# Kernel tuning notes

Hardware: AMD Instinct MI355X
Metric: run time of the kernel (lower is better)

Reference implementation:

```python
import jax, jax.numpy as jnp
import numpy as np

N_NODES = 50000
N_EDGES = 800000
NUM_FEATURES = 128
HIDDEN = 128


def _gcn_conv(x, src, dst, norm, W, b, num_nodes):
    # x: [N, F_in], W: [F_in, F_out]
    h = x @ W                              # dense transform first (PyG order)
    msg = h[src] * norm[:, None]           # gather + per-edge scale
    out = jax.ops.segment_sum(msg, dst, num_segments=num_nodes)  # scatter-add
    return out + b


def _prep_edges(edge_index, num_nodes):
    # add self loops
    loop = jnp.arange(num_nodes, dtype=edge_index.dtype)
    src = jnp.concatenate([edge_index[0], loop])
    dst = jnp.concatenate([edge_index[1], loop])
    # symmetric normalization deg^{-1/2}[src] * deg^{-1/2}[dst]
    deg = jax.ops.segment_sum(jnp.ones_like(dst, dtype=jnp.float32), dst,
                              num_segments=num_nodes)
    dinv = jnp.where(deg > 0, jax.lax.rsqrt(deg), 0.0)
    norm = dinv[src] * dinv[dst]
    return src, dst, norm


def setup_inputs() -> dict:
    key = jax.random.key(0)
    ks = jax.random.split(key, 5)
    s1 = 1.0 / np.sqrt(NUM_FEATURES)
    s2 = 1.0 / np.sqrt(HIDDEN)
    return {
        "x": jax.random.normal(ks[0], (N_NODES, NUM_FEATURES), jnp.float32),
        "edge_index": jax.random.randint(ks[1], (2, N_EDGES), 0, N_NODES,
                                         dtype=jnp.int64),
        "W1": jax.random.normal(ks[2], (NUM_FEATURES, HIDDEN), jnp.float32) * s1,
        "b1": jnp.zeros((HIDDEN,), jnp.float32),
        "W2": jax.random.normal(ks[3], (HIDDEN, HIDDEN), jnp.float32) * s2,
        "b2": jnp.zeros((HIDDEN,), jnp.float32),
        "Wout": jax.random.normal(ks[4], (HIDDEN, 1), jnp.float32) * s2,
        "bout": jnp.zeros((1,), jnp.float32),
    }


def reference(x, edge_index, W1, b1, W2, b2, Wout, bout):
    num_nodes = x.shape[0]
    src, dst, norm = _prep_edges(edge_index, num_nodes)
    h = _gcn_conv(x, src, dst, norm, W1, b1, num_nodes)
    h = jax.nn.relu(h)
    h = _gcn_conv(h, src, dst, norm, W2, b2, num_nodes)
    h = jax.nn.relu(h)
    return jax.nn.sigmoid(h @ Wout + bout)
```

## Files before the change

### kernel.cpp

```cpp
#include <hip/hip_runtime.h>
#include <math.h>

#define NN 50000
#define NE 800000
#define NBUK 196
#define PBLK 256
#define EPB (NE / PBLK)

typedef __attribute__((ext_vector_type(8))) short bf16x8;
typedef __attribute__((ext_vector_type(4))) float f32x4;

__device__ __forceinline__ unsigned short f2b(float f) {
  union { float f; unsigned u; } v; v.f = f;
  unsigned r = v.u + 0x7FFF + ((v.u >> 16) & 1);
  return (unsigned short)(r >> 16);
}
__device__ __forceinline__ float plo(unsigned v) {
  union { unsigned u; float f; } t; t.u = v << 16; return t.f;
}
__device__ __forceinline__ float phi(unsigned v) {
  union { unsigned u; float f; } t; t.u = v & 0xFFFF0000u; return t.f;
}

__device__ __forceinline__ int edge_val(const void* ei, long long idx, int is64) {
  if (is64) return (int)((const long long*)ei)[idx];
  return ((const int*)ei)[idx];
}

__global__ __launch_bounds__(256) void k_phist(const void* __restrict__ ei,
                                               int* __restrict__ bh) {
  __shared__ int hist[NBUK];
  __shared__ int sflag;
  if (threadIdx.x < 64) {
    unsigned v = ((const unsigned*)ei)[2 * threadIdx.x + 1];
    unsigned long long m = __ballot(v == 0u);
    if (threadIdx.x == 0) sflag = (m == ~0ull) ? 1 : 0;
  }
  if (threadIdx.x < NBUK) hist[threadIdx.x] = 0;
  __syncthreads();
  int is64 = sflag;
  int base = blockIdx.x * EPB;
  for (int e = base + threadIdx.x; e < base + EPB; e += 256) {
    int d = edge_val(ei, (long long)NE + e, is64);
    atomicAdd(&hist[d >> 8], 1);
  }
  __syncthreads();
  if (threadIdx.x < NBUK) bh[threadIdx.x * PBLK + blockIdx.x] = hist[threadIdx.x];
}

__global__ __launch_bounds__(256) void k_pscanA(int* __restrict__ bh,
                                                int* __restrict__ colsum) {
  __shared__ int sh[256];
  int k = blockIdx.x, t = threadIdx.x;
  int v = bh[k * PBLK + t];
  sh[t] = v;
  __syncthreads();
  for (int s = 1; s < 256; s <<= 1) {
    int u = (t >= s) ? sh[t - s] : 0;
    __syncthreads();
    sh[t] += u;
    __syncthreads();
  }
  bh[k * PBLK + t] = sh[t] - v;
  if (t == 255) colsum[k] = sh[255];
}

__global__ __launch_bounds__(256) void k_pscanB(const int* __restrict__ colsum,
                                                int* __restrict__ bstart) {
  __shared__ int sh[256];
  int t = threadIdx.x;
  sh[t] = (t < NBUK) ? colsum[t] : 0;
  __syncthreads();
  for (int s = 1; s < 256; s <<= 1) {
    int u = (t >= s) ? sh[t - s] : 0;
    __syncthreads();
    sh[t] += u;
    __syncthreads();
  }
  if (t <= NBUK) bstart[t] = (t == 0) ? 0 : sh[t - 1];
}

__global__ __launch_bounds__(256) void k_pscat(const void* __restrict__ ei,
                                               const int* __restrict__ bh,
                                               const int* __restrict__ bstart,
                                               int2* __restrict__ epair) {
  __shared__ int cur[NBUK];
  __shared__ int sflag;
  if (threadIdx.x < 64) {
    unsigned v = ((const unsigned*)ei)[2 * threadIdx.x + 1];
    unsigned long long m = __ballot(v == 0u);
    if (threadIdx.x == 0) sflag = (m == ~0ull) ? 1 : 0;
  }
  if (threadIdx.x < NBUK)
    cur[threadIdx.x] = bstart[threadIdx.x] + bh[threadIdx.x * PBLK + blockIdx.x];
  __syncthreads();
  int is64 = sflag;
  int base = blockIdx.x * EPB;
  for (int e = base + threadIdx.x; e < base + EPB; e += 256) {
    int d = edge_val(ei, (long long)NE + e, is64);
    int s = edge_val(ei, e, is64);
    int p = atomicAdd(&cur[d >> 8], 1);
    epair[p] = make_int2(s, d);
  }
}

__global__ __launch_bounds__(256) void k_boff(const int2* __restrict__ epair,
                                              const int* __restrict__ bstart,
                                              int* __restrict__ off,
                                              float* __restrict__ dinv) {
  __shared__ int hist[256];
  int k = blockIdx.x, t = threadIdx.x;
  hist[t] = 0;
  __syncthreads();
  int e0 = bstart[k], e1 = bstart[k + 1];
  for (int e = e0 + t; e < e1; e += 256)
    atomicAdd(&hist[epair[e].y & 255], 1);
  __syncthreads();
  int myc = hist[t];
  for (int s = 1; s < 256; s <<= 1) {
    int u = (t >= s) ? hist[t - s] : 0;
    __syncthreads();
    hist[t] += u;
    __syncthreads();
  }
  int node = k * 256 + t;
  if (node < NN) {
    off[node] = e0 + hist[t] - myc;
    dinv[node] = rsqrtf((float)(myc + 1));
  }
  if (k == 0 && t == 0) off[NN] = NE;
}

__global__ __launch_bounds__(256) void k_bfill(const int2* __restrict__ epair,
                                               const int* __restrict__ bstart,
                                               const int* __restrict__ off,
                                               int* __restrict__ csr) {
  __shared__ int cur[256];
  int k = blockIdx.x, t = threadIdx.x;
  int node = k * 256 + t;
  cur[t] = (node < NN) ? off[node] : 0;
  __syncthreads();
  int e0 = bstart[k], e1 = bstart[k + 1];
  for (int e = e0 + t; e < e1; e += 256) {
    int2 p2 = epair[e];
    int p = atomicAdd(&cur[p2.y & 255], 1);
    csr[p] = p2.x;
  }
}

__global__ __launch_bounds__(256) void k_wt2(const float* __restrict__ W1,
                                             const float* __restrict__ W2,
                                             unsigned short* __restrict__ Wt1,
                                             unsigned short* __restrict__ Wt2) {
  int i = blockIdx.x * 256 + threadIdx.x;
  int sel = i >> 14;
  int j = i & 16383;
  int k = j >> 7, n = j & 127;
  const float* W = sel ? W2 : W1;
  unsigned short* Wt = sel ? Wt2 : Wt1;
  Wt[n * 128 + k] = f2b(W[j]);
}

template <int A_F32>
__global__ __launch_bounds__(256, 2) void k_mgemm(const void* __restrict__ Ap,
                                                  const unsigned short* __restrict__ Wt,
                                                  unsigned short* __restrict__ Out,
                                                  int M) {
  int wid  = (blockIdx.x * blockDim.x + threadIdx.x) >> 6;
  int lane = threadIdx.x & 63;
  int nw   = (gridDim.x * blockDim.x) >> 6;
  int r  = lane & 15;
  int kg = lane >> 4;
  bf16x8 wf[8][4];
#pragma unroll
  for (int n = 0; n < 8; ++n)
#pragma unroll
    for (int kk = 0; kk < 4; ++kk)
      wf[n][kk] = *(const bf16x8*)&Wt[(n * 16 + r) * 128 + kk * 32 + kg * 8];
  int nstr = M >> 4;
  for (int s = wid; s < nstr; s += nw) {
    int row = s * 16 + r;
    bf16x8 xf[4];
    if (A_F32) {
      const float* Ar = (const float*)Ap + (long long)row * 128 + kg * 8;
#pragma unroll
      for (int kk = 0; kk < 4; ++kk) {
        float4 lo4 = *(const float4*)(Ar + kk * 32);
        float4 hi4 = *(const float4*)(Ar + kk * 32 + 4);
        bf16x8 t;
        t[0] = (short)f2b(lo4.x); t[1] = (short)f2b(lo4.y);
        t[2] = (short)f2b(lo4.z); t[3] = (short)f2b(lo4.w);
        t[4] = (short)f2b(hi4.x); t[5] = (short)f2b(hi4.y);
        t[6] = (short)f2b(hi4.z); t[7] = (short)f2b(hi4.w);
        xf[kk] = t;
      }
    } else {
      const unsigned short* Ar = (const unsigned short*)Ap + (long long)row * 128 + kg * 8;
#pragma unroll
      for (int kk = 0; kk < 4; ++kk)
        xf[kk] = *(const bf16x8*)(Ar + kk * 32);
    }
    f32x4 acc[8];
#pragma unroll
    for (int n = 0; n < 8; ++n) acc[n] = (f32x4){0.f, 0.f, 0.f, 0.f};
#pragma unroll
    for (int kk = 0; kk < 4; ++kk)
#pragma unroll
      for (int n = 0; n < 8; ++n)
        acc[n] = __builtin_amdgcn_mfma_f32_16x16x32_bf16(wf[n][kk], xf[kk], acc[n], 0, 0, 0);
    unsigned short* Or = Out + (long long)row * 128 + kg * 4;
#pragma unroll
    for (int n = 0; n < 8; ++n) {
      uint2 o;
      o.x = (unsigned)f2b(acc[n][0]) | ((unsigned)f2b(acc[n][1]) << 16);
      o.y = (unsigned)f2b(acc[n][2]) | ((unsigned)f2b(acc[n][3]) << 16);
      *(uint2*)(Or + n * 16) = o;
    }
  }
}

template <int FINAL>
__global__ __launch_bounds__(256) void k_agg(const unsigned short* __restrict__ Tb,
                                             const int* __restrict__ off,
                                             const int* __restrict__ csr,
                                             const float* __restrict__ dinv,
                                             const float* __restrict__ bias,
                                             const float* __restrict__ wout,
                                             const float* __restrict__ bout,
                                             void* __restrict__ outp) {
  const unsigned* Tw = (const unsigned*)Tb;
  int wid  = (blockIdx.x * blockDim.x + threadIdx.x) >> 6;
  int lane = threadIdx.x & 63;
  int nw   = (gridDim.x * blockDim.x) >> 6;
  float blo = bias[2 * lane], bhi = bias[2 * lane + 1];
  float wlo = 0.f, whi = 0.f;
  if (FINAL) { wlo = wout[2 * lane]; whi = wout[2 * lane + 1]; }
  for (int d = wid; d < NN; d += nw) {
    float dv = dinv[d];
    int e0 = off[d], e1 = off[d + 1];
    unsigned vs = Tw[d * 64 + lane];
    float a0 = dv * plo(vs);
    float a1 = dv * phi(vs);
    int e = e0;
    int e8 = e0 + ((e1 - e0) & ~7);
    for (; e < e8; e += 8) {
      int   si[8]; float wi[8]; unsigned vi[8];
#pragma unroll
      for (int q = 0; q < 8; ++q) si[q] = csr[e + q];
#pragma unroll
      for (int q = 0; q < 8; ++q) wi[q] = dinv[si[q]];
#pragma unroll
      for (int q = 0; q < 8; ++q) vi[q] = Tw[si[q] * 64 + lane];
#pragma unroll
      for (int q = 0; q < 8; ++q) {
        a0 = fmaf(wi[q], plo(vi[q]), a0);
        a1 = fmaf(wi[q], phi(vi[q]), a1);
      }
    }
    for (; e < e1; ++e) {
      int s = csr[e];
      float w = dinv[s];
      unsigned v = Tw[s * 64 + lane];
      a0 = fmaf(w, plo(v), a0);
      a1 = fmaf(w, phi(v), a1);
    }
    a0 = fmaxf(fmaf(a0, dv, blo), 0.f);
    a1 = fmaxf(fmaf(a1, dv, bhi), 0.f);
    if (FINAL) {
      float rsum = a0 * wlo + a1 * whi;
#pragma unroll
      for (int s2p = 32; s2p > 0; s2p >>= 1) rsum += __shfl_xor(rsum, s2p, 64);
      if (lane == 0) ((float*)outp)[d] = 1.f / (1.f + __expf(-(rsum + bout[0])));
    } else {
      unsigned o = (unsigned)f2b(a0) | ((unsigned)f2b(a1) << 16);
      ((unsigned*)outp)[d * 64 + lane] = o;
    }
  }
}

extern "C" void kernel_launch(void* const* d_in, const int* in_sizes, int n_in,
                              void* d_out, int out_size, void* d_ws, size_t ws_size,
                              hipStream_t stream) {
  const float* x  = (const float*)d_in[0];
  const void*  ei = d_in[1];
  const float* W1 = (const float*)d_in[2];
  const float* b1 = (const float*)d_in[3];
  const float* W2 = (const float*)d_in[4];
  const float* b2 = (const float*)d_in[5];
  const float* Wo = (const float*)d_in[6];
  const float* bo = (const float*)d_in[7];
  float* out = (float*)d_out;

  char* p = (char*)d_ws;
  auto alloc = [&](size_t bytes) {
    char* r = p;
    p += (bytes + 511) & ~(size_t)511;
    return r;
  };
  int*   bh     = (int*)alloc(sizeof(int) * NBUK * PBLK);
  int*   colsum = (int*)alloc(sizeof(int) * NBUK);
  int*   bstart = (int*)alloc(sizeof(int) * (NBUK + 1));
  int*   off    = (int*)alloc(sizeof(int) * (NN + 1));
  float* dinv   = (float*)alloc(sizeof(float) * NN);
  int*   csr    = (int*)alloc(sizeof(int) * NE);
  unsigned short* Wt1 = (unsigned short*)alloc(sizeof(short) * 128 * 128);
  unsigned short* Wt2 = (unsigned short*)alloc(sizeof(short) * 128 * 128);
  unsigned short* T   = (unsigned short*)alloc(sizeof(short) * (size_t)NN * 128);
  unsigned short* H   = (unsigned short*)alloc(sizeof(short) * (size_t)NN * 128);
  int2* epair = (int2*)T;

  k_phist<<<PBLK, 256, 0, stream>>>(ei, bh);
  k_pscanA<<<NBUK, 256, 0, stream>>>(bh, colsum);
  k_pscanB<<<1, 256, 0, stream>>>(colsum, bstart);
  k_pscat<<<PBLK, 256, 0, stream>>>(ei, bh, bstart, epair);
  k_boff<<<NBUK, 256, 0, stream>>>(epair, bstart, off, dinv);
  k_bfill<<<NBUK, 256, 0, stream>>>(epair, bstart, off, csr);
  k_wt2<<<128, 256, 0, stream>>>(W1, W2, Wt1, Wt2);

  k_mgemm<1><<<512, 256, 0, stream>>>(x, Wt1, T, NN);
  k_agg<0><<<2048, 256, 0, stream>>>(T, off, csr, dinv, b1, nullptr, nullptr, H);
  k_mgemm<0><<<512, 256, 0, stream>>>(H, Wt2, T, NN);
  k_agg<1><<<2048, 256, 0, stream>>>(T, off, csr, dinv, b2, Wo, bo, out);
}
```

Measured before the change: 241.7 us.

## Pre-scale GEMM rows by dinv, pack CSR to 16-bit, split aggregation across half-waves

Each GEMM output row is now multiplied by dinv[row], so aggregation no longer gathers dinv per edge. CSR indices are stored as 16-bit values, and the offset and fill kernels are merged into one, with 32-bit packed edge pairs. Aggregation processes two edges per wave, one per half-wave with 8-byte loads per lane, then combines the halves with a shuffle. The risk is that 16-bit indices cannot address all 50000 nodes, since values above 65535 would be truncated, and node ids fit only because NN < 65536.

```diff
diff --git a/kernel.cpp b/kernel.cpp
--- a/kernel.cpp
+++ b/kernel.cpp
@@ -83,7 +83,7 @@
 __global__ __launch_bounds__(256) void k_pscat(const void* __restrict__ ei,
                                                const int* __restrict__ bh,
                                                const int* __restrict__ bstart,
-                                               int2* __restrict__ epair) {
+                                               unsigned* __restrict__ epk) {
   __shared__ int cur[NBUK];
   __shared__ int sflag;
   if (threadIdx.x < 64) {
@@ -100,21 +100,23 @@
     int d = edge_val(ei, (long long)NE + e, is64);
     int s = edge_val(ei, e, is64);
     int p = atomicAdd(&cur[d >> 8], 1);
-    epair[p] = make_int2(s, d);
-  }
-}
-
-__global__ __launch_bounds__(256) void k_boff(const int2* __restrict__ epair,
-                                              const int* __restrict__ bstart,
-                                              int* __restrict__ off,
-                                              float* __restrict__ dinv) {
+    epk[p] = (unsigned)s | ((unsigned)(d & 255) << 16);
+  }
+}
+
+__global__ __launch_bounds__(256) void k_bofffill(const unsigned* __restrict__ epk,
+                                                  const int* __restrict__ bstart,
+                                                  int* __restrict__ off,
+                                                  float* __restrict__ dinv,
+                                                  unsigned short* __restrict__ csr16) {
   __shared__ int hist[256];
+  __shared__ int cur[256];
   int k = blockIdx.x, t = threadIdx.x;
   hist[t] = 0;
   __syncthreads();
   int e0 = bstart[k], e1 = bstart[k + 1];
   for (int e = e0 + t; e < e1; e += 256)
-    atomicAdd(&hist[epair[e].y & 255], 1);
+    atomicAdd(&hist[(epk[e] >> 16) & 255], 1);
   __syncthreads();
   int myc = hist[t];
   for (int s = 1; s < 256; s <<= 1) {
@@ -123,29 +125,20 @@
     hist[t] += u;
     __syncthreads();
   }
+  int excl = hist[t] - myc;
   int node = k * 256 + t;
   if (node < NN) {
-    off[node] = e0 + hist[t] - myc;
+    off[node] = e0 + excl;
     dinv[node] = rsqrtf((float)(myc + 1));
   }
+  cur[t] = e0 + excl;
+  __syncthreads();
+  for (int e = e0 + t; e < e1; e += 256) {
+    unsigned pk = epk[e];
+    int p = atomicAdd(&cur[(pk >> 16) & 255], 1);
+    csr16[p] = (unsigned short)(pk & 0xFFFFu);
+  }
   if (k == 0 && t == 0) off[NN] = NE;
-}
-
-__global__ __launch_bounds__(256) void k_bfill(const int2* __restrict__ epair,
-                                               const int* __restrict__ bstart,
-                                               const int* __restrict__ off,
-                                               int* __restrict__ csr) {
-  __shared__ int cur[256];
-  int k = blockIdx.x, t = threadIdx.x;
-  int node = k * 256 + t;
-  cur[t] = (node < NN) ? off[node] : 0;
-  __syncthreads();
-  int e0 = bstart[k], e1 = bstart[k + 1];
-  for (int e = e0 + t; e < e1; e += 256) {
-    int2 p2 = epair[e];
-    int p = atomicAdd(&cur[p2.y & 255], 1);
-    csr[p] = p2.x;
-  }
 }
 
 __global__ __launch_bounds__(256) void k_wt2(const float* __restrict__ W1,
@@ -164,6 +157,7 @@
 template <int A_F32>
 __global__ __launch_bounds__(256, 2) void k_mgemm(const void* __restrict__ Ap,
                                                   const unsigned short* __restrict__ Wt,
+                                                  const float* __restrict__ dinv,
                                                   unsigned short* __restrict__ Out,
                                                   int M) {
   int wid  = (blockIdx.x * blockDim.x + threadIdx.x) >> 6;
@@ -208,12 +202,13 @@
 #pragma unroll
       for (int n = 0; n < 8; ++n)
         acc[n] = __builtin_amdgcn_mfma_f32_16x16x32_bf16(wf[n][kk], xf[kk], acc[n], 0, 0, 0);
+    float dv = dinv[row];
     unsigned short* Or = Out + (long long)row * 128 + kg * 4;
 #pragma unroll
     for (int n = 0; n < 8; ++n) {
       uint2 o;
-      o.x = (unsigned)f2b(acc[n][0]) | ((unsigned)f2b(acc[n][1]) << 16);
-      o.y = (unsigned)f2b(acc[n][2]) | ((unsigned)f2b(acc[n][3]) << 16);
+      o.x = (unsigned)f2b(acc[n][0] * dv) | ((unsigned)f2b(acc[n][1] * dv) << 16);
+      o.y = (unsigned)f2b(acc[n][2] * dv) | ((unsigned)f2b(acc[n][3] * dv) << 16);
       *(uint2*)(Or + n * 16) = o;
     }
   }
@@ -222,58 +217,76 @@
 template <int FINAL>
 __global__ __launch_bounds__(256) void k_agg(const unsigned short* __restrict__ Tb,
                                              const int* __restrict__ off,
-                                             const int* __restrict__ csr,
+                                             const unsigned short* __restrict__ csr16,
                                              const float* __restrict__ dinv,
                                              const float* __restrict__ bias,
                                              const float* __restrict__ wout,
                                              const float* __restrict__ bout,
                                              void* __restrict__ outp) {
-  const unsigned* Tw = (const unsigned*)Tb;
+  const uint2* Tw2 = (const uint2*)Tb;
   int wid  = (blockIdx.x * blockDim.x + threadIdx.x) >> 6;
   int lane = threadIdx.x & 63;
+  int half = lane >> 5;
+  int li   = lane & 31;
   int nw   = (gridDim.x * blockDim.x) >> 6;
-  float blo = bias[2 * lane], bhi = bias[2 * lane + 1];
-  float wlo = 0.f, whi = 0.f;
-  if (FINAL) { wlo = wout[2 * lane]; whi = wout[2 * lane + 1]; }
+  float4 b4 = ((const float4*)bias)[li];
+  float4 w4 = make_float4(0.f, 0.f, 0.f, 0.f);
+  if (FINAL) w4 = ((const float4*)wout)[li];
   for (int d = wid; d < NN; d += nw) {
+    int e0 = off[d], e1 = off[d + 1];
+    int np  = (e1 - e0) >> 1;
+    int rem = (e1 - e0) & 1;
+    int s_init = half ? (rem ? (int)csr16[e1 - 1] : -1) : d;
+    float a0 = 0.f, a1 = 0.f, a2 = 0.f, a3 = 0.f;
+    if (s_init >= 0) {
+      uint2 vv = Tw2[s_init * 32 + li];
+      a0 = plo(vv.x); a1 = phi(vv.x); a2 = plo(vv.y); a3 = phi(vv.y);
+    }
+    int st = 0;
+    int base = e0 + half;
+    for (; st + 4 <= np; st += 4) {
+      int s0 = csr16[base + 2 * st];
+      int s1 = csr16[base + 2 * st + 2];
+      int s2 = csr16[base + 2 * st + 4];
+      int s3 = csr16[base + 2 * st + 6];
+      uint2 v0 = Tw2[s0 * 32 + li];
+      uint2 v1 = Tw2[s1 * 32 + li];
+      uint2 v2 = Tw2[s2 * 32 + li];
+      uint2 v3 = Tw2[s3 * 32 + li];
+      a0 += plo(v0.x); a1 += phi(v0.x); a2 += plo(v0.y); a3 += phi(v0.y);
+      a0 += plo(v1.x); a1 += phi(v1.x); a2 += plo(v1.y); a3 += phi(v1.y);
+      a0 += plo(v2.x); a1 += phi(v2.x); a2 += plo(v2.y); a3 += phi(v2.y);
+      a0 += plo(v3.x); a1 += phi(v3.x); a2 += plo(v3.y); a3 += phi(v3.y);
+    }
+    for (; st < np; ++st) {
+      int s = csr16[base + 2 * st];
+      uint2 vv = Tw2[s * 32 + li];
+      a0 += plo(vv.x); a1 += phi(vv.x); a2 += plo(vv.y); a3 += phi(vv.y);
+    }
+    a0 += __shfl_xor(a0, 32, 64);
+    a1 += __shfl_xor(a1, 32, 64);
+    a2 += __shfl_xor(a2, 32, 64);
+    a3 += __shfl_xor(a3, 32, 64);
     float dv = dinv[d];
-    int e0 = off[d], e1 = off[d + 1];
-    unsigned vs = Tw[d * 64 + lane];
-    float a0 = dv * plo(vs);
-    float a1 = dv * phi(vs);
-    int e = e0;
-    int e8 = e0 + ((e1 - e0) & ~7);
-    for (; e < e8; e += 8) {
-      int   si[8]; float wi[8]; unsigned vi[8];
-#pragma unroll
-      for (int q = 0; q < 8; ++q) si[q] = csr[e + q];
-#pragma unroll
-      for (int q = 0; q < 8; ++q) wi[q] = dinv[si[q]];
-#pragma unroll
-      for (int q = 0; q < 8; ++q) vi[q] = Tw[si[q] * 64 + lane];
-#pragma unroll
-      for (int q = 0; q < 8; ++q) {
-        a0 = fmaf(wi[q], plo(vi[q]), a0);
-        a1 = fmaf(wi[q], phi(vi[q]), a1);
+    a0 = fmaxf(fmaf(a0, dv, b4.x), 0.f);
+    a1 = fmaxf(fmaf(a1, dv, b4.y), 0.f);
+    a2 = fmaxf(fmaf(a2, dv, b4.z), 0.f);
+    a3 = fmaxf(fmaf(a3, dv, b4.w), 0.f);
+    if (FINAL) {
+      float r = a0 * w4.x + a1 * w4.y + a2 * w4.z + a3 * w4.w;
+      r += __shfl_xor(r, 16, 64);
+      r += __shfl_xor(r, 8, 64);
+      r += __shfl_xor(r, 4, 64);
+      r += __shfl_xor(r, 2, 64);
+      r += __shfl_xor(r, 1, 64);
+      if (lane == 0) ((float*)outp)[d] = 1.f / (1.f + __expf(-(r + bout[0])));
+    } else {
+      if (half == 0) {
+        uint2 o;
+        o.x = (unsigned)f2b(a0) | ((unsigned)f2b(a1) << 16);
+        o.y = (unsigned)f2b(a2) | ((unsigned)f2b(a3) << 16);
+        ((uint2*)outp)[d * 32 + li] = o;
       }
-    }
-    for (; e < e1; ++e) {
-      int s = csr[e];
-      float w = dinv[s];
-      unsigned v = Tw[s * 64 + lane];
-      a0 = fmaf(w, plo(v), a0);
-      a1 = fmaf(w, phi(v), a1);
-    }
-    a0 = fmaxf(fmaf(a0, dv, blo), 0.f);
-    a1 = fmaxf(fmaf(a1, dv, bhi), 0.f);
-    if (FINAL) {
-      float rsum = a0 * wlo + a1 * whi;
-#pragma unroll
-      for (int s2p = 32; s2p > 0; s2p >>= 1) rsum += __shfl_xor(rsum, s2p, 64);
-      if (lane == 0) ((float*)outp)[d] = 1.f / (1.f + __expf(-(rsum + bout[0])));
-    } else {
-      unsigned o = (unsigned)f2b(a0) | ((unsigned)f2b(a1) << 16);
-      ((unsigned*)outp)[d * 64 + lane] = o;
     }
   }
 }
@@ -302,23 +315,22 @@
   int*   bstart = (int*)alloc(sizeof(int) * (NBUK + 1));
   int*   off    = (int*)alloc(sizeof(int) * (NN + 1));
   float* dinv   = (float*)alloc(sizeof(float) * NN);
-  int*   csr    = (int*)alloc(sizeof(int) * NE);
+  unsigned short* csr16 = (unsigned short*)alloc(sizeof(short) * NE);
   unsigned short* Wt1 = (unsigned short*)alloc(sizeof(short) * 128 * 128);
   unsigned short* Wt2 = (unsigned short*)alloc(sizeof(short) * 128 * 128);
   unsigned short* T   = (unsigned short*)alloc(sizeof(short) * (size_t)NN * 128);
   unsigned short* H   = (unsigned short*)alloc(sizeof(short) * (size_t)NN * 128);
-  int2* epair = (int2*)T;
+  unsigned* epk = (unsigned*)T;
 
   k_phist<<<PBLK, 256, 0, stream>>>(ei, bh);
   k_pscanA<<<NBUK, 256, 0, stream>>>(bh, colsum);
   k_pscanB<<<1, 256, 0, stream>>>(colsum, bstart);
-  k_pscat<<<PBLK, 256, 0, stream>>>(ei, bh, bstart, epair);
-  k_boff<<<NBUK, 256, 0, stream>>>(epair, bstart, off, dinv);
-  k_bfill<<<NBUK, 256, 0, stream>>>(epair, bstart, off, csr);
+  k_pscat<<<PBLK, 256, 0, stream>>>(ei, bh, bstart, epk);
+  k_bofffill<<<NBUK, 256, 0, stream>>>(epk, bstart, off, dinv, csr16);
   k_wt2<<<128, 256, 0, stream>>>(W1, W2, Wt1, Wt2);
 
-  k_mgemm<1><<<512, 256, 0, stream>>>(x, Wt1, T, NN);
-  k_agg<0><<<2048, 256, 0, stream>>>(T, off, csr, dinv, b1, nullptr, nullptr, H);
-  k_mgemm<0><<<512, 256, 0, stream>>>(H, Wt2, T, NN);
-  k_agg<1><<<2048, 256, 0, stream>>>(T, off, csr, dinv, b2, Wo, bo, out);
-}
+  k_mgemm<1><<<512, 256, 0, stream>>>(x, Wt1, dinv, T, NN);
+  k_agg<0><<<2048, 256, 0, stream>>>(T, off, csr16, dinv, b1, nullptr, nullptr, H);
+  k_mgemm<0><<<512, 256, 0, stream>>>(H, Wt2, dinv, T, NN);
+  k_agg<1><<<2048, 256, 0, stream>>>(T, off, csr16, dinv, b2, Wo, bo, out);
+}
```

Measured after the change: 213.4 us, median of 2. 1.13x faster.
